# Performance work log

Measured on AMD Instinct MI355X. Metric: run time of the kernel, lower is better.

## Reference

```python
import jax, jax.numpy as jnp
import numpy as np

B, T, V, E, H = 32, 512, 20000, 300, 512


def setup_inputs() -> dict:
    key = jax.random.key(0)
    k1, k2, k3, k4 = jax.random.split(key, 4)
    tokens = jax.random.randint(k1, (B, T), 0, V, dtype=jnp.int32)
    emb = jax.random.normal(k2, (V, E), dtype=jnp.float32)
    # Keras LSTM: kernel [E, 4H], recurrent_kernel [H, 4H], bias [4H]
    W = jax.random.normal(k3, (E, 4 * H), dtype=jnp.float32) * (1.0 / np.sqrt(E))
    U = jax.random.normal(k4, (H, 4 * H), dtype=jnp.float32) * (1.0 / np.sqrt(H))
    b = jnp.zeros((4 * H,), dtype=jnp.float32)
    return {"tokens": tokens, "emb": emb, "W": W, "U": U, "b": b}


def _lstm_last_state(x, W, U, b):
    # x: [B, T, E].  Gate order (Keras): i, f, g(candidate), o.
    h0 = jnp.zeros((x.shape[0], H), dtype=x.dtype)
    c0 = jnp.zeros((x.shape[0], H), dtype=x.dtype)
    # Precompute input projections for all timesteps: [T, B, 4H]
    xz = jnp.einsum('bte,eg->tbg', x, W) + b

    def step(carry, xz_t):
        h, c = carry
        z = xz_t + h @ U                      # [B, 4H]
        i, f, g, o = jnp.split(z, 4, axis=-1)
        i = jax.nn.sigmoid(i)
        f = jax.nn.sigmoid(f)
        g = jnp.tanh(g)
        o = jax.nn.sigmoid(o)
        c = f * c + i * g
        h = o * jnp.tanh(c)
        return (h, c), None

    (h, c), _ = jax.lax.scan(step, (h0, c0), xz)
    return h, c


def reference(tokens, emb, W, U, b):
    x = emb[tokens]                            # [B, T, E] embedding lookup
    hidden, cell = _lstm_last_state(x, W, U, b)
    return (hidden, cell)                      # Encoder returns (hidden, cell)
```

## Files before the change

### kernel.cpp

```cpp
#include <hip/hip_runtime.h>
#include <hip/hip_bf16.h>

typedef unsigned short u16;
typedef unsigned int u32;
typedef unsigned long long u64;
typedef short  s16x8 __attribute__((ext_vector_type(8)));
typedef float  f32x4 __attribute__((ext_vector_type(4)));
typedef u32    u32x4 __attribute__((ext_vector_type(4)));

#define T_STEPS 512
#define BATCH   32
#define HID     512
#define EMBD    300
#define NGATE   2048

#define XZ_OFF   0ull
#define XZ_BYTES (512ull*32*2048*4)
#define UB_OFF   (XZ_OFF + XZ_BYTES)
#define UB_BYTES (2048ull*512*2)
#define WT_OFF   (UB_OFF + UB_BYTES)
#define WT_BYTES (2048ull*320*2)
#define HB_OFF   (WT_OFF + WT_BYTES)
#define HB_BYTES (2ull*8192*4)

__device__ inline u16 f2b(float f) {
  u32 u = __builtin_bit_cast(u32, f);
  return (u16)((u + 0x7fffu + ((u >> 16) & 1u)) >> 16);
}

__device__ inline void st32_agent(u32* p, u32 v) {
  __hip_atomic_store(p, v, __ATOMIC_RELAXED, __HIP_MEMORY_SCOPE_AGENT);
}

__global__ __launch_bounds__(64) void pack_w(const float* __restrict__ W, u16* __restrict__ wt) {
  int n = blockIdx.x;
  for (int i = 0; i < 5; ++i) {
    int k = i * 64 + threadIdx.x;
    float v = (k < EMBD) ? W[(size_t)k * NGATE + n] : 0.f;
    u32 off = ((u32)(2 * k)) ^ (((u32)(n & 7)) << 4);
    *(u16*)((char*)wt + (size_t)n * 640 + off) = f2b(v);
  }
}

__global__ __launch_bounds__(64) void pack_u(const float* __restrict__ U, u16* __restrict__ ub) {
  int blk = blockIdx.x;
  int w = blk >> 6, nl = blk & 63;
  int gcol = (nl & 3) * 512 + w * 16 + (nl >> 2);
  for (int i = 0; i < 8; ++i) {
    int k = i * 64 + threadIdx.x;
    float v = U[(size_t)k * NGATE + gcol];
    u32 off = ((u32)(2 * k)) ^ (((u32)(nl & 7)) << 4);
    *(u16*)((char*)ub + (size_t)blk * 1024 + off) = f2b(v);
  }
}

__global__ __launch_bounds__(256) void xz_gemm(const int* __restrict__ tokens,
                                               const float* __restrict__ emb,
                                               const u16* __restrict__ wt,
                                               const float* __restrict__ bias,
                                               float* __restrict__ xz) {
  extern __shared__ char smem[];
  const int tid = threadIdx.x;
  const int lane = tid & 63, wv = tid >> 6;
  const int m0 = (blockIdx.x >> 5) * 64;
  const int n0 = (blockIdx.x & 31) * 64;

  {
    int row = tid >> 2, q = tid & 3;
    int tok = tokens[m0 + row];
    const float* er = emb + (size_t)tok * EMBD;
    for (int i = 0; i < 10; ++i) {
      int k = q * 80 + i * 8;
      float4 lo = {0, 0, 0, 0}, hi = {0, 0, 0, 0};
      if (k <= 296) lo = *(const float4*)(er + k);
      if (k <= 292) hi = *(const float4*)(er + k + 4);
      u16 u[8] = {f2b(lo.x), f2b(lo.y), f2b(lo.z), f2b(lo.w),
                  f2b(hi.x), f2b(hi.y), f2b(hi.z), f2b(hi.w)};
      int kc = q * 10 + i;
      *(uint4*)(smem + kc * 1040 + row * 16) = *(uint4*)u;
    }
  }
  {
    const uint4* src = (const uint4*)((const char*)wt + (size_t)n0 * 640);
    for (int i = 0; i < 10; ++i)
      *(uint4*)(smem + 41600 + (i * 256 + tid) * 16) = src[i * 256 + tid];
  }
  __syncthreads();

  const int mq = wv >> 1, nq = wv & 1;
  const int arow = lane & 15, kq4 = lane >> 4;
  f32x4 acc[2][2] = {};
#pragma unroll
  for (int ks = 0; ks < 10; ++ks) {
    s16x8 af[2], bfr[2];
#pragma unroll
    for (int mt = 0; mt < 2; ++mt) {
      int row = mq * 32 + mt * 16 + arow;
      int kc = ks * 4 + kq4;
      af[mt] = *(const s16x8*)(smem + kc * 1040 + row * 16);
    }
#pragma unroll
    for (int nt = 0; nt < 2; ++nt) {
      int nl = nq * 32 + nt * 16 + arow;
      u32 kb = (u32)(ks * 64 + (kq4 << 4));
      bfr[nt] = *(const s16x8*)(smem + 41600 + nl * 640 + (kb ^ (((u32)(nl & 7)) << 4)));
    }
#pragma unroll
    for (int mt = 0; mt < 2; ++mt)
#pragma unroll
      for (int nt = 0; nt < 2; ++nt)
        acc[mt][nt] = __builtin_amdgcn_mfma_f32_16x16x32_bf16(af[mt], bfr[nt], acc[mt][nt], 0, 0, 0);
  }
#pragma unroll
  for (int mt = 0; mt < 2; ++mt)
#pragma unroll
    for (int nt = 0; nt < 2; ++nt) {
      int gn = n0 + nq * 32 + nt * 16 + arow;
      float bv = bias[gn];
      int g = gn >> 9, j = gn & 511;
      size_t inner = (size_t)((j >> 4) * 64 + g * 16 + (j & 15));
#pragma unroll
      for (int r = 0; r < 4; ++r) {
        int gm = m0 + mq * 32 + mt * 16 + (kq4 << 2) + r;
        int tt = gm & 511, bb = gm >> 9;
        xz[(size_t)(tt * 32 + bb) * 2048 + inner] = acc[mt][nt][r] + bv;
      }
    }
}

__global__ __launch_bounds__(256) void lstm_persist(const float* __restrict__ xz,
                                                    const u16* __restrict__ ub,
                                                    u32* __restrict__ hbuf,
                                                    float* __restrict__ out) {
  extern __shared__ char smem[];
  char*  hl   = smem + 65536;
  float* zlds = (float*)(smem + 98304);
  const int tid = threadIdx.x;
  const int lane = tid & 63, wv = tid >> 6;
  const int wg = blockIdx.x;

  {
    const uint4* src = (const uint4*)(ub + (size_t)wg * 32768);
    uint4* dst = (uint4*)smem;
    for (int i = 0; i < 16; ++i) dst[i * 256 + tid] = src[i * 256 + tid];
  }
  __syncthreads();

  const int b_g = tid & 31;
  const int pp  = tid >> 5;
  const int arow = lane & 15, kq = lane >> 4;
  const int nl = wv * 16 + (lane & 15);
  const u32 bswz = ((u32)(nl & 7)) << 4;
  const int j0 = wg * 16;
  float c0 = 0.f, c1 = 0.f;

  const u32 vo0 = (u32)(tid * 16 + 1 * 4096), vo1 = (u32)(tid * 16 + 3 * 4096);
  const u32 vo2 = (u32)(tid * 16 + 5 * 4096), vo3 = (u32)(tid * 16 + 7 * 4096);
  const u32 hrow0 = (u32)(tid >> 6);
  const u32 hcolb = (u32)((tid & 63) * 16);

  float xzv[2][4];
  {
    const float* p = xz + (size_t)b_g * 2048 + wg * 64 + 2 * pp;
#pragma unroll
    for (int g = 0; g < 4; ++g) {
      float2 v = *(const float2*)(p + g * 16);
      xzv[0][g] = v.x; xzv[1][g] = v.y;
    }
  }

  for (int t = 0; t < T_STEPS; ++t) {
    if (t > 0) {
      u32 tg = (((u32)t >> 1) + 1u) & 3u;
      u32 pat = (tg & 1u) | ((tg >> 1) << 16);
      const u64 sb = (u64)(uintptr_t)hbuf + (u64)((t & 1) * 32768);
      u32x4 q0, q1, q2, q3, q4, q5, q6, q7;
      int tries = 0;
      for (;;) {
        asm volatile(
          "global_load_dwordx4 %0, %8, %12 offset:-4096 sc0 sc1\n\t"
          "global_load_dwordx4 %1, %8, %12 sc0 sc1\n\t"
          "global_load_dwordx4 %2, %9, %12 offset:-4096 sc0 sc1\n\t"
          "global_load_dwordx4 %3, %9, %12 sc0 sc1\n\t"
          "global_load_dwordx4 %4, %10, %12 offset:-4096 sc0 sc1\n\t"
          "global_load_dwordx4 %5, %10, %12 sc0 sc1\n\t"
          "global_load_dwordx4 %6, %11, %12 offset:-4096 sc0 sc1\n\t"
          "global_load_dwordx4 %7, %11, %12 sc0 sc1\n\t"
          "s_waitcnt vmcnt(0)"
          : "=&v"(q0), "=&v"(q1), "=&v"(q2), "=&v"(q3),
            "=&v"(q4), "=&v"(q5), "=&v"(q6), "=&v"(q7)
          : "v"(vo0), "v"(vo1), "v"(vo2), "v"(vo3), "s"(sb)
          : "memory");
        u32 x0 = (q0.x ^ pat) | (q0.y ^ pat) | (q0.z ^ pat) | (q0.w ^ pat);
        u32 x1 = (q1.x ^ pat) | (q1.y ^ pat) | (q1.z ^ pat) | (q1.w ^ pat);
        u32 x2 = (q2.x ^ pat) | (q2.y ^ pat) | (q2.z ^ pat) | (q2.w ^ pat);
        u32 x3 = (q3.x ^ pat) | (q3.y ^ pat) | (q3.z ^ pat) | (q3.w ^ pat);
        u32 x4 = (q4.x ^ pat) | (q4.y ^ pat) | (q4.z ^ pat) | (q4.w ^ pat);
        u32 x5 = (q5.x ^ pat) | (q5.y ^ pat) | (q5.z ^ pat) | (q5.w ^ pat);
        u32 x6 = (q6.x ^ pat) | (q6.y ^ pat) | (q6.z ^ pat) | (q6.w ^ pat);
        u32 x7 = (q7.x ^ pat) | (q7.y ^ pat) | (q7.z ^ pat) | (q7.w ^ pat);
        u32 bad = (x0 | x1 | x2 | x3 | x4 | x5 | x6 | x7) & 0x00010001u;
        if (bad == 0 || ++tries > 65536) break;
        __builtin_amdgcn_s_sleep(1);
      }
#define HW(L, Q) { u32 r_ = hrow0 + 4u * (L);                                  \
        u32 off_ = r_ * 1024u + (hcolb ^ ((r_ & 7u) << 4));                    \
        *(u32x4*)(hl + off_) = (Q); }
      HW(0, q0) HW(1, q1) HW(2, q2) HW(3, q3)
      HW(4, q4) HW(5, q5) HW(6, q6) HW(7, q7)
#undef HW
    }
    __syncthreads();

    if (t > 0) {
      f32x4 acc0 = {0, 0, 0, 0}, acc1 = {0, 0, 0, 0};
      const u32 aswz = ((u32)(arow & 7)) << 4;
#pragma unroll
      for (int ks = 0; ks < 16; ++ks) {
        u32 kb = (u32)(ks * 64 + (kq << 4));
        s16x8 a0 = *(const s16x8*)(hl + arow * 1024 + (kb ^ aswz));
        s16x8 a1 = *(const s16x8*)(hl + (arow + 16) * 1024 + (kb ^ aswz));
        s16x8 bb = *(const s16x8*)(smem + nl * 1024 + (kb ^ bswz));
        acc0 = __builtin_amdgcn_mfma_f32_16x16x32_bf16(a0, bb, acc0, 0, 0, 0);
        acc1 = __builtin_amdgcn_mfma_f32_16x16x32_bf16(a1, bb, acc1, 0, 0, 0);
      }
      int rb = kq * 4;
#pragma unroll
      for (int r = 0; r < 4; ++r) {
        zlds[(rb + r) * 67 + nl] = acc0[r];
        zlds[(rb + r + 16) * 67 + nl] = acc1[r];
      }
    }
    __syncthreads();

    float hov[2], cov[2];
    float zv[8] = {0, 0, 0, 0, 0, 0, 0, 0};
    if (t > 0) {
      const float* zp = &zlds[b_g * 67 + 8 * pp];
#pragma unroll
      for (int m = 0; m < 8; ++m) zv[m] = zp[m];
    }
#pragma unroll
    for (int e = 0; e < 2; ++e) {
      float zi = zv[4 * e + 0] + xzv[e][0];
      float zf = zv[4 * e + 1] + xzv[e][1];
      float zg = zv[4 * e + 2] + xzv[e][2];
      float zo = zv[4 * e + 3] + xzv[e][3];
      float ig = 1.f / (1.f + __expf(-zi));
      float fg = 1.f / (1.f + __expf(-zf));
      float gg = 1.f - 2.f / (__expf(2.f * zg) + 1.f);
      float og = 1.f / (1.f + __expf(-zo));
      float cc = e ? c1 : c0;
      cc = fg * cc + ig * gg;
      float hh = og * (1.f - 2.f / (__expf(2.f * cc) + 1.f));
      if (e) c1 = cc; else c0 = cc;
      hov[e] = hh; cov[e] = cc;
    }

    if (t < T_STEPS - 1) {
      u32 tg2 = (((u32)(t + 1) >> 1) + 1u) & 3u;
      u32 val = ((u32)(f2b(hov[0]) & 0xFFFEu) | (tg2 & 1u)) |
                ((((u32)(f2b(hov[1]) & 0xFFFEu)) | ((tg2 >> 1) & 1u)) << 16);
      st32_agent(&hbuf[(size_t)((t + 1) & 1) * 8192 + b_g * 256 + wg * 8 + pp], val);
      {
        const float* p = xz + ((size_t)(t + 1) * 32 + b_g) * 2048 + wg * 64 + 2 * pp;
#pragma unroll
        for (int g = 0; g < 4; ++g) {
          float2 v = *(const float2*)(p + g * 16);
          xzv[0][g] = v.x; xzv[1][g] = v.y;
        }
      }
    } else {
#pragma unroll
      for (int e = 0; e < 2; ++e) {
        int jl = 2 * pp + e;
        out[b_g * 512 + j0 + jl] = hov[e];
        out[16384 + b_g * 512 + j0 + jl] = cov[e];
      }
    }
  }
}

extern "C" void kernel_launch(void* const* d_in, const int* in_sizes, int n_in,
                              void* d_out, int out_size, void* d_ws, size_t ws_size,
                              hipStream_t stream) {
  const int*   tokens = (const int*)d_in[0];
  const float* emb    = (const float*)d_in[1];
  const float* W      = (const float*)d_in[2];
  const float* U      = (const float*)d_in[3];
  const float* bias   = (const float*)d_in[4];
  float* out = (float*)d_out;
  char*  ws  = (char*)d_ws;

  float* xz   = (float*)(ws + XZ_OFF);
  u16*   ub   = (u16*)(ws + UB_OFF);
  u16*   wt   = (u16*)(ws + WT_OFF);
  u32*   hbuf = (u32*)(ws + HB_OFF);

  hipMemsetAsync(hbuf, 0, HB_BYTES, stream);
  pack_w<<<2048, 64, 0, stream>>>(W, wt);
  pack_u<<<2048, 64, 0, stream>>>(U, ub);
  xz_gemm<<<8192, 256, 82560, stream>>>(tokens, emb, wt, bias, xz);
  lstm_persist<<<32, 256, 106880, stream>>>(xz, ub, hbuf, out);
}
```

Measured before the change: 1.742 ms.

## Swap MFMA operands so gate accumulators land in-thread, dropping LDS z round-trip

Swaps the MFMA operands (U as A, h as B) so each lane's accumulator holds all four gates for one hidden unit and batch row. The LSTM cell update can then read directly from registers, which removes the per-step LDS write/read of z and one __syncthreads barrier in the serial recurrence. Packing the next h requires a cross-lane shuffle to pair batch rows into the same 32-bit word, and the xz loads become scalar instead of float2. LDS allocation shrinks accordingly.

```diff
diff --git a/kernel.cpp b/kernel.cpp
--- a/kernel.cpp
+++ b/kernel.cpp
@@ -133,8 +133,7 @@
                                                     u32* __restrict__ hbuf,
                                                     float* __restrict__ out) {
   extern __shared__ char smem[];
-  char*  hl   = smem + 65536;
-  float* zlds = (float*)(smem + 98304);
+  char* hl = smem + 65536;
   const int tid = threadIdx.x;
   const int lane = tid & 63, wv = tid >> 6;
   const int wg = blockIdx.x;
@@ -144,14 +143,13 @@
     uint4* dst = (uint4*)smem;
     for (int i = 0; i < 16; ++i) dst[i * 256 + tid] = src[i * 256 + tid];
   }
-  __syncthreads();
-
-  const int b_g = tid & 31;
-  const int pp  = tid >> 5;
+
   const int arow = lane & 15, kq = lane >> 4;
-  const int nl = wv * 16 + (lane & 15);
+  const int nl = wv * 16 + arow;
   const u32 bswz = ((u32)(nl & 7)) << 4;
+  const u32 aswz = ((u32)(arow & 7)) << 4;
   const int j0 = wg * 16;
+  const int jl = 4 * wv + kq;
   float c0 = 0.f, c1 = 0.f;
 
   const u32 vo0 = (u32)(tid * 16 + 1 * 4096), vo1 = (u32)(tid * 16 + 3 * 4096);
@@ -159,15 +157,19 @@
   const u32 hrow0 = (u32)(tid >> 6);
   const u32 hcolb = (u32)((tid & 63) * 16);
 
+  const int pb   = (kq & 1) ? (arow + 16) : arow;
+  const u32 pidx = (u32)(pb * 256 + wg * 8 + 2 * wv + (kq >> 1));
+
   float xzv[2][4];
   {
-    const float* p = xz + (size_t)b_g * 2048 + wg * 64 + 2 * pp;
+    const float* p = xz + (size_t)arow * 2048 + wg * 64 + jl;
 #pragma unroll
     for (int g = 0; g < 4; ++g) {
-      float2 v = *(const float2*)(p + g * 16);
-      xzv[0][g] = v.x; xzv[1][g] = v.y;
-    }
-  }
+      xzv[0][g] = p[g * 16];
+      xzv[1][g] = p[16 * 2048 + g * 16];
+    }
+  }
+  __syncthreads();
 
   for (int t = 0; t < T_STEPS; ++t) {
     if (t > 0) {
@@ -212,40 +214,27 @@
     }
     __syncthreads();
 
+    f32x4 acc0 = {0, 0, 0, 0}, acc1 = {0, 0, 0, 0};
     if (t > 0) {
-      f32x4 acc0 = {0, 0, 0, 0}, acc1 = {0, 0, 0, 0};
-      const u32 aswz = ((u32)(arow & 7)) << 4;
 #pragma unroll
       for (int ks = 0; ks < 16; ++ks) {
         u32 kb = (u32)(ks * 64 + (kq << 4));
-        s16x8 a0 = *(const s16x8*)(hl + arow * 1024 + (kb ^ aswz));
-        s16x8 a1 = *(const s16x8*)(hl + (arow + 16) * 1024 + (kb ^ aswz));
-        s16x8 bb = *(const s16x8*)(smem + nl * 1024 + (kb ^ bswz));
-        acc0 = __builtin_amdgcn_mfma_f32_16x16x32_bf16(a0, bb, acc0, 0, 0, 0);
-        acc1 = __builtin_amdgcn_mfma_f32_16x16x32_bf16(a1, bb, acc1, 0, 0, 0);
-      }
-      int rb = kq * 4;
-#pragma unroll
-      for (int r = 0; r < 4; ++r) {
-        zlds[(rb + r) * 67 + nl] = acc0[r];
-        zlds[(rb + r + 16) * 67 + nl] = acc1[r];
-      }
-    }
-    __syncthreads();
+        s16x8 uu = *(const s16x8*)(smem + nl * 1024 + (kb ^ bswz));
+        s16x8 h0 = *(const s16x8*)(hl + arow * 1024 + (kb ^ aswz));
+        s16x8 h1 = *(const s16x8*)(hl + (arow + 16) * 1024 + (kb ^ aswz));
+        acc0 = __builtin_amdgcn_mfma_f32_16x16x32_bf16(uu, h0, acc0, 0, 0, 0);
+        acc1 = __builtin_amdgcn_mfma_f32_16x16x32_bf16(uu, h1, acc1, 0, 0, 0);
+      }
+    }
 
     float hov[2], cov[2];
-    float zv[8] = {0, 0, 0, 0, 0, 0, 0, 0};
-    if (t > 0) {
-      const float* zp = &zlds[b_g * 67 + 8 * pp];
-#pragma unroll
-      for (int m = 0; m < 8; ++m) zv[m] = zp[m];
-    }
 #pragma unroll
     for (int e = 0; e < 2; ++e) {
-      float zi = zv[4 * e + 0] + xzv[e][0];
-      float zf = zv[4 * e + 1] + xzv[e][1];
-      float zg = zv[4 * e + 2] + xzv[e][2];
-      float zo = zv[4 * e + 3] + xzv[e][3];
+      f32x4 zr = e ? acc1 : acc0;
+      float zi = zr[0] + xzv[e][0];
+      float zf = zr[1] + xzv[e][1];
+      float zg = zr[2] + xzv[e][2];
+      float zo = zr[3] + xzv[e][3];
       float ig = 1.f / (1.f + __expf(-zi));
       float fg = 1.f / (1.f + __expf(-zf));
       float gg = 1.f - 2.f / (__expf(2.f * zg) + 1.f);
@@ -258,25 +247,27 @@
     }
 
     if (t < T_STEPS - 1) {
+      u32 pk = (u32)f2b(hov[0]) | ((u32)f2b(hov[1]) << 16);
+      u32 pr = (u32)__shfl_xor((int)pk, 16, 64);
+      u32 val = (kq & 1) ? ((pr >> 16) | (pk & 0xFFFF0000u))
+                         : ((pk & 0xFFFFu) | (pr << 16));
       u32 tg2 = (((u32)(t + 1) >> 1) + 1u) & 3u;
-      u32 val = ((u32)(f2b(hov[0]) & 0xFFFEu) | (tg2 & 1u)) |
-                ((((u32)(f2b(hov[1]) & 0xFFFEu)) | ((tg2 >> 1) & 1u)) << 16);
-      st32_agent(&hbuf[(size_t)((t + 1) & 1) * 8192 + b_g * 256 + wg * 8 + pp], val);
+      val = (val & 0xFFFEFFFEu) | (tg2 & 1u) | ((tg2 >> 1) << 16);
+      st32_agent(&hbuf[(size_t)((t + 1) & 1) * 8192 + pidx], val);
       {
-        const float* p = xz + ((size_t)(t + 1) * 32 + b_g) * 2048 + wg * 64 + 2 * pp;
+        const float* p = xz + ((size_t)(t + 1) * 32 + arow) * 2048 + wg * 64 + jl;
 #pragma unroll
         for (int g = 0; g < 4; ++g) {
-          float2 v = *(const float2*)(p + g * 16);
-          xzv[0][g] = v.x; xzv[1][g] = v.y;
+          xzv[0][g] = p[g * 16];
+          xzv[1][g] = p[16 * 2048 + g * 16];
         }
       }
     } else {
-#pragma unroll
-      for (int e = 0; e < 2; ++e) {
-        int jl = 2 * pp + e;
-        out[b_g * 512 + j0 + jl] = hov[e];
-        out[16384 + b_g * 512 + j0 + jl] = cov[e];
-      }
+      int j = j0 + jl;
+      out[arow * 512 + j]                 = hov[0];
+      out[(arow + 16) * 512 + j]          = hov[1];
+      out[16384 + arow * 512 + j]         = cov[0];
+      out[16384 + (arow + 16) * 512 + j]  = cov[1];
     }
   }
 }
@@ -301,5 +292,5 @@
   pack_w<<<2048, 64, 0, stream>>>(W, wt);
   pack_u<<<2048, 64, 0, stream>>>(U, ub);
   xz_gemm<<<8192, 256, 82560, stream>>>(tokens, emb, wt, bias, xz);
-  lstm_persist<<<32, 256, 106880, stream>>>(xz, ub, hbuf, out);
-}
+  lstm_persist<<<32, 256, 98304, stream>>>(xz, ub, hbuf, out);
+}
```

Result: slower. 1.790 ms (+2.8%).
